# Kernel optimization log

Hardware: AMD Instinct MI355X
Metric: run time of the kernel (lower is better)

Reference implementation:

```python
import jax, jax.numpy as jnp
import numpy as np

N = 100000   # nodes
E = 300000   # directed edges
NG = 4096    # graphs in batch
F_IN = 22
HID = 128


def setup_inputs() -> dict:
    key = jax.random.key(0)
    ks = jax.random.split(key, 32)
    s = 0.05
    inp = {
        "x": jax.random.normal(ks[0], (N, F_IN), jnp.float32),
        "edge_index": jax.random.randint(ks[1], (2, E), 0, N),
        "batch": jnp.sort(jax.random.randint(ks[2], (N,), 0, NG)),
        # GAT layer 1: 22 -> 4 heads x 32
        "W1": jax.random.normal(ks[3], (F_IN, HID), jnp.float32) * s,
        "as1": jax.random.normal(ks[4], (4, 32), jnp.float32) * s,
        "ad1": jax.random.normal(ks[5], (4, 32), jnp.float32) * s,
        "b1": jnp.zeros((HID,), jnp.float32),
        "g1": jnp.ones((HID,), jnp.float32),
        "be1": jnp.zeros((HID,), jnp.float32),
        # GAT layer 2: 128 -> 4 heads x 32
        "W2": jax.random.normal(ks[6], (HID, HID), jnp.float32) * s,
        "as2": jax.random.normal(ks[7], (4, 32), jnp.float32) * s,
        "ad2": jax.random.normal(ks[8], (4, 32), jnp.float32) * s,
        "b2": jnp.zeros((HID,), jnp.float32),
        "g2": jnp.ones((HID,), jnp.float32),
        "be2": jnp.zeros((HID,), jnp.float32),
        # GAT layer 3: 128 -> 1 head x 128
        "W3": jax.random.normal(ks[9], (HID, HID), jnp.float32) * s,
        "as3": jax.random.normal(ks[10], (1, HID), jnp.float32) * s,
        "ad3": jax.random.normal(ks[11], (1, HID), jnp.float32) * s,
        "b3": jnp.zeros((HID,), jnp.float32),
        "g3": jnp.ones((HID,), jnp.float32),
        "be3": jnp.zeros((HID,), jnp.float32),
        # MLP head
        "fw1": jax.random.normal(ks[12], (HID, 64), jnp.float32) * s,
        "fb1": jnp.zeros((64,), jnp.float32),
        "fw2": jax.random.normal(ks[13], (64, 1), jnp.float32) * s,
        "fb2": jnp.zeros((1,), jnp.float32),
    }
    return inp


def reference(x, edge_index, batch, W1, as1, ad1, b1, g1, be1,
              W2, as2, ad2, b2, g2, be2, W3, as3, ad3, b3, g3, be3,
              fw1, fb1, fw2, fb2):
    n = x.shape[0]
    sl = jnp.arange(n)
    src = jnp.concatenate([edge_index[0], sl])  # PyG GATConv adds self-loops
    dst = jnp.concatenate([edge_index[1], sl])

    def gat(h_in, W, a_s, a_d, b):
        H, C = a_s.shape
        h = (h_in @ W).reshape(n, H, C)                      # [N,H,C]
        al_s = jnp.einsum('nhc,hc->nh', h, a_s)              # per-node src score
        al_d = jnp.einsum('nhc,hc->nh', h, a_d)
        e = jax.nn.leaky_relu(al_s[src] + al_d[dst], 0.2)    # [Etot,H]
        emax = jax.ops.segment_max(e, dst, num_segments=n)
        ex = jnp.exp(e - emax[dst])
        den = jax.ops.segment_sum(ex, dst, num_segments=n)
        alpha = ex / (den[dst] + 1e-16)                       # segment softmax over in-edges
        msg = h[src] * alpha[:, :, None]                      # [Etot,H,C]
        out = jax.ops.segment_sum(msg, dst, num_segments=n)
        return out.reshape(n, H * C) + b

    def bn(h, g, be):
        m = h.mean(0)
        v = h.var(0)
        return (h - m) * jax.lax.rsqrt(v + 1e-5) * g + be

    h = jax.nn.relu(bn(gat(x, W1, as1, ad1, b1), g1, be1))
    h = jax.nn.relu(bn(gat(h, W2, as2, ad2, b2), g2, be2))
    h = jax.nn.relu(bn(gat(h, W3, as3, ad3, b3), g3, be3))

    # global mean pool over graphs
    s = jax.ops.segment_sum(h, batch, num_segments=NG)
    cnt = jax.ops.segment_sum(jnp.ones((n,), h.dtype), batch, num_segments=NG)
    pooled = s / jnp.maximum(cnt, 1.0)[:, None]

    z = jax.nn.relu(pooled @ fw1 + fb1)
    return z @ fw2 + fb2
```

## Files before the change

### kernel.cpp

```cpp
#include <hip/hip_runtime.h>

#define N_NODES 100000
#define N_EDGES 300000
#define N_ETOT  400000
#define NGRAPH  4096
#define HID     128
#define NBLK_SCAN 391
#define PNPB    32
#define STATS_BLOCKS 512
#define NSLICE  64

typedef __attribute__((ext_vector_type(8))) short short8;
typedef __attribute__((ext_vector_type(8))) ushort ushort8;
typedef __attribute__((ext_vector_type(4))) float f32x4;

__device__ __forceinline__ ushort f2bf(float f) {
    union { float f; unsigned u; } x; x.f = f;
    unsigned r = x.u + 0x7FFF + ((x.u >> 16) & 1);
    return (ushort)(r >> 16);
}

__device__ __forceinline__ float bf2f(ushort v) {
    union { unsigned u; float f; } t;
    t.u = ((unsigned)v) << 16;
    return t.f;
}

__device__ __forceinline__ float2 bf2f2(unsigned v) {
    union { unsigned u; float f; } lo, hi;
    lo.u = v << 16;
    hi.u = v & 0xFFFF0000u;
    return make_float2(lo.f, hi.f);
}

__global__ __launch_bounds__(256) void setup_kernel(
    const float* __restrict__ x,
    const float* __restrict__ W1, const float* __restrict__ W2, const float* __restrict__ W3,
    ushort* __restrict__ Wt1, ushort* __restrict__ Wt2, ushort* __restrict__ Wt3,
    ushort* __restrict__ Xb, float* __restrict__ sums_sl, int* __restrict__ counts,
    float* __restrict__ pooled)
{
    const int i = blockIdx.x * 256 + threadIdx.x;
    if (i < 16384) {
        int c = i >> 7, k = i & 127;
        Wt2[c * 128 + k] = f2bf(W2[k * 128 + c]);
    } else if (i < 32768) {
        int j = i - 16384; int c = j >> 7, k = j & 127;
        Wt3[c * 128 + k] = f2bf(W3[k * 128 + c]);
    } else if (i < 36864) {
        int j = i - 32768; int c = j >> 5, k = j & 31;
        Wt1[c * 32 + k] = (k < 22) ? f2bf(W1[k * 128 + c]) : (ushort)0;
    } else if (i < 36864 + N_NODES * 32) {
        int j = i - 36864; int n = j >> 5, k = j & 31;
        Xb[j] = (k < 22) ? f2bf(x[n * 22 + k]) : (ushort)0;
    } else if (i < 36864 + N_NODES * 32 + NSLICE * 256) {
        sums_sl[i - (36864 + N_NODES * 32)] = 0.f;
    } else if (i < 36864 + N_NODES * 32 + NSLICE * 256 + N_NODES) {
        counts[i - (36864 + N_NODES * 32 + NSLICE * 256)] = 0;
    } else if (i < 36864 + N_NODES * 32 + NSLICE * 256 + N_NODES + NGRAPH * HID + NGRAPH) {
        pooled[i - (36864 + N_NODES * 32 + NSLICE * 256 + N_NODES)] = 0.f;
    }
}
#define SETUP_TOT (36864 + N_NODES * 32 + NSLICE * 256 + N_NODES + NGRAPH * HID + NGRAPH)

template<int K, bool PRE_BN, int HH>
__global__ __launch_bounds__(256) void mfma_gemm_kernel(
    const ushort* __restrict__ Ab, const ushort* __restrict__ Wt,
    const float* __restrict__ scale, const float* __restrict__ shift,
    const float* __restrict__ avs, const float* __restrict__ avd,
    ushort* __restrict__ Cb, float* __restrict__ als, float* __restrict__ ald, int M)
{
    constexpr int BK  = 32;
    constexpr int LDK = 40;
    constexpr int NT  = K / BK;
    __shared__ ushort Asm[128 * LDK];
    __shared__ ushort Bsm[128 * LDK];
    __shared__ float  ps[128][4], pd[128][4];

    const int tid  = threadIdx.x;
    const int wave = tid >> 6;
    const int lane = tid & 63;
    const int ln   = lane & 15;
    const int quad = lane >> 4;
    const int wr0  = (wave >> 1) * 64;
    const int wc0  = (wave & 1) * 64;
    const int row0 = blockIdx.x * 128;

    f32x4 acc[4][4] = {};

    for (int t = 0; t < NT; ++t) {
        const int k0 = t * BK;
        #pragma unroll
        for (int q = 0; q < 2; ++q) {
            const int chunk = tid + q * 256;
            const int r = chunk >> 2, seg = chunk & 3;
            short8 v = *(const short8*)&Ab[(size_t)(row0 + r) * K + k0 + seg * 8];
            if constexpr (PRE_BN) {
                const int cc = k0 + seg * 8;
                #pragma unroll
                for (int i = 0; i < 8; ++i) {
                    float f = bf2f((ushort)v[i]);
                    f = fmaxf(f * scale[cc + i] + shift[cc + i], 0.f);
                    v[i] = (short)f2bf(f);
                }
            }
            *(short8*)&Asm[r * LDK + seg * 8] = v;
        }
        #pragma unroll
        for (int q = 0; q < 2; ++q) {
            const int chunk = tid + q * 256;
            const int c = chunk >> 2, seg = chunk & 3;
            short8 v = *(const short8*)&Wt[(size_t)c * K + k0 + seg * 8];
            *(short8*)&Bsm[c * LDK + seg * 8] = v;
        }
        __syncthreads();
        short8 af[4], bf[4];
        #pragma unroll
        for (int i = 0; i < 4; ++i) {
            af[i] = *(const short8*)&Asm[(wr0 + i * 16 + ln) * LDK + quad * 8];
            bf[i] = *(const short8*)&Bsm[(wc0 + i * 16 + ln) * LDK + quad * 8];
        }
        #pragma unroll
        for (int tr = 0; tr < 4; ++tr)
            #pragma unroll
            for (int tc = 0; tc < 4; ++tc)
                acc[tr][tc] = __builtin_amdgcn_mfma_f32_16x16x32_bf16(
                    af[tr], bf[tc], acc[tr][tc], 0, 0, 0);
        __syncthreads();
    }

    #pragma unroll
    for (int tr = 0; tr < 4; ++tr)
        #pragma unroll
        for (int rg = 0; rg < 4; ++rg) {
            const int gr = row0 + wr0 + tr * 16 + quad * 4 + rg;
            if (gr < M) {
                #pragma unroll
                for (int tc = 0; tc < 4; ++tc)
                    Cb[(size_t)gr * HID + wc0 + tc * 16 + ln] = f2bf(acc[tr][tc][rg]);
            }
        }

    #pragma unroll
    for (int tr = 0; tr < 4; ++tr)
      #pragma unroll
      for (int rg = 0; rg < 4; ++rg) {
        float sA = 0.f, sB = 0.f, dA = 0.f, dB = 0.f;
        #pragma unroll
        for (int tc = 0; tc < 4; ++tc) {
            const int col = wc0 + tc * 16 + ln;
            const float v = acc[tr][tc][rg];
            if (tc < 2) { sA += v * avs[col]; dA += v * avd[col]; }
            else        { sB += v * avs[col]; dB += v * avd[col]; }
        }
        #pragma unroll
        for (int m = 1; m < 16; m <<= 1) {
            sA += __shfl_xor(sA, m); sB += __shfl_xor(sB, m);
            dA += __shfl_xor(dA, m); dB += __shfl_xor(dB, m);
        }
        if (ln == 0) {
            const int rl = wr0 + tr * 16 + quad * 4 + rg;
            const int h0 = (wave & 1) * 2;
            ps[rl][h0] = sA; ps[rl][h0 + 1] = sB;
            pd[rl][h0] = dA; pd[rl][h0 + 1] = dB;
        }
      }
    __syncthreads();
    {
        const int r  = tid & 127;
        const int gr = row0 + r;
        if (gr < M) {
            if (tid < 128) {
                if (HH == 4) {
                    #pragma unroll
                    for (int h = 0; h < 4; ++h) als[gr * 4 + h] = ps[r][h];
                } else als[gr] = ps[r][0] + ps[r][1] + ps[r][2] + ps[r][3];
            } else {
                if (HH == 4) {
                    #pragma unroll
                    for (int h = 0; h < 4; ++h) ald[gr * 4 + h] = pd[r][h];
                } else ald[gr] = pd[r][0] + pd[r][1] + pd[r][2] + pd[r][3];
            }
        }
    }
}

__global__ void hist_kernel(const int* __restrict__ ei, int* __restrict__ counts) {
    int e = blockIdx.x * blockDim.x + threadIdx.x;
    if (e >= N_ETOT) return;
    int dst = (e < N_EDGES) ? ei[N_EDGES + e] : e - N_EDGES;
    atomicAdd(&counts[dst], 1);
}

__global__ __launch_bounds__(256) void scanA_kernel(
    const int* __restrict__ counts, int* __restrict__ rowptr, int* __restrict__ bsum)
{
    __shared__ int ls[256];
    const int t = threadIdx.x;
    const int i = blockIdx.x * 256 + t;
    const int v = (i < N_NODES) ? counts[i] : 0;
    ls[t] = v; __syncthreads();
    #pragma unroll
    for (int off = 1; off < 256; off <<= 1) {
        int add = (t >= off) ? ls[t - off] : 0;
        __syncthreads();
        ls[t] += add;
        __syncthreads();
    }
    if (i < N_NODES) rowptr[i] = ls[t] - v;
    if (t == 255) bsum[blockIdx.x] = ls[255];
}

__global__ __launch_bounds__(512) void scanB_kernel(int* __restrict__ bsum)
{
    __shared__ int ls[512];
    const int t = threadIdx.x;
    const int v = (t < NBLK_SCAN) ? bsum[t] : 0;
    ls[t] = v; __syncthreads();
    #pragma unroll
    for (int off = 1; off < 512; off <<= 1) {
        int add = (t >= off) ? ls[t - off] : 0;
        __syncthreads();
        ls[t] += add;
        __syncthreads();
    }
    if (t < NBLK_SCAN) bsum[t] = ls[t] - v;
}

__global__ void scanC_kernel(int* __restrict__ rowptr, const int* __restrict__ bsum,
                             int* __restrict__ cursor)
{
    int i = blockIdx.x * 256 + threadIdx.x;
    if (i < N_NODES) {
        int v = rowptr[i] + bsum[blockIdx.x];
        rowptr[i] = v;
        cursor[i] = v;
    }
    if (i == 0) rowptr[N_NODES] = N_ETOT;
}

__global__ void scatter_kernel(const int* __restrict__ ei, int* __restrict__ cursor,
                               int* __restrict__ psrc)
{
    int e = blockIdx.x * blockDim.x + threadIdx.x;
    if (e >= N_ETOT) return;
    int src, dst;
    if (e < N_EDGES) { src = ei[e]; dst = ei[N_EDGES + e]; }
    else             { src = dst = e - N_EDGES; }
    int pos = atomicAdd(&cursor[dst], 1);
    psrc[pos] = src;
}

template<int HH>
__global__ __launch_bounds__(256) void agg_kernel(
    const ushort* __restrict__ H, const float* __restrict__ als,
    const float* __restrict__ ald, const int* __restrict__ rowptr,
    const int* __restrict__ psrc, ushort* __restrict__ Outb)
{
    const int tid  = threadIdx.x;
    const int node = blockIdx.x * 4 + (tid >> 6);
    const int lane = tid & 63;
    const int grp  = lane >> 4;
    const int cl   = lane & 15;
    const int hd   = (HH == 4) ? (cl >> 2) : 0;
    const int r0 = rowptr[node];
    const int r1 = rowptr[node + 1];
    const float aldh = (HH == 4) ? ald[node * 4 + hd] : ald[node];

    float den = 0.f;
    float acc[8] = {};
    for (int p = r0 + grp; p < r1; p += 4) {
        const int src = psrc[p];
        float v = ((HH == 4) ? als[src * 4 + hd] : als[src]) + aldh;
        v = (v > 0.f) ? v : 0.2f * v;
        const float ex = __expf(v);
        const uint4 hv = *(const uint4*)&H[(size_t)src * HID + cl * 8];
        const float2 h0 = bf2f2(hv.x), h1 = bf2f2(hv.y);
        const float2 h2 = bf2f2(hv.z), h3 = bf2f2(hv.w);
        acc[0] += ex * h0.x; acc[1] += ex * h0.y;
        acc[2] += ex * h1.x; acc[3] += ex * h1.y;
        acc[4] += ex * h2.x; acc[5] += ex * h2.y;
        acc[6] += ex * h3.x; acc[7] += ex * h3.y;
        den += ex;
    }
    #pragma unroll
    for (int m = 16; m < 64; m <<= 1) {
        den += __shfl_xor(den, m);
        #pragma unroll
        for (int i = 0; i < 8; ++i) acc[i] += __shfl_xor(acc[i], m);
    }
    if (grp == 0) {
        const float inv = 1.f / (den + 1e-16f);
        ushort8 o;
        #pragma unroll
        for (int i = 0; i < 8; ++i) o[i] = f2bf(acc[i] * inv);
        *(ushort8*)&Outb[(size_t)node * HID + cl * 8] = o;
    }
}

__global__ __launch_bounds__(256) void bn_stats_kernel(
    const ushort* __restrict__ X, float* __restrict__ sums_sl)
{
    __shared__ float ls[16][128], lq[16][128];
    const int tid = threadIdx.x;
    const int ro  = tid >> 4;
    const int ci  = tid & 15;
    const int c0  = ci * 8;
    const int rpb = (N_NODES + STATS_BLOCKS - 1) / STATS_BLOCKS;
    const int r0  = blockIdx.x * rpb;
    const int r1  = min(r0 + rpb, N_NODES);

    float s[8] = {}, q[8] = {};
    for (int r = r0 + ro; r < r1; r += 16) {
        const ushort8 v = *(const ushort8*)&X[(size_t)r * HID + c0];
        #pragma unroll
        for (int j = 0; j < 8; ++j) {
            const float f = bf2f(v[j]);
            s[j] += f; q[j] += f * f;
        }
    }
    #pragma unroll
    for (int j = 0; j < 8; ++j) { ls[ro][c0 + j] = s[j]; lq[ro][c0 + j] = q[j]; }
    __syncthreads();
    const int half = tid >> 7;
    const int c    = tid & 127;
    float acc = 0.f;
    if (half == 0) {
        #pragma unroll
        for (int k = 0; k < 16; ++k) acc += ls[k][c];
    } else {
        #pragma unroll
        for (int k = 0; k < 16; ++k) acc += lq[k][c];
    }
    atomicAdd(&sums_sl[(blockIdx.x & (NSLICE - 1)) * 256 + tid], acc);
}

__global__ __launch_bounds__(256) void bn_finalize_kernel(
    float* __restrict__ sums_sl,
    const float* __restrict__ g, const float* __restrict__ be,
    float* __restrict__ scale, float* __restrict__ shift)
{
    __shared__ float red[256];
    const int tid = threadIdx.x;
    float s = 0.f;
    for (int b = 0; b < NSLICE; ++b) {
        s += sums_sl[b * 256 + tid];
        sums_sl[b * 256 + tid] = 0.f;
    }
    red[tid] = s;
    __syncthreads();
    if (tid < 128) {
        const float m = red[tid] * (1.f / N_NODES);
        const float v = red[tid + 128] * (1.f / N_NODES) - m * m;
        const float sc = g[tid] * rsqrtf(v + 1e-5f);
        scale[tid] = sc;
        shift[tid] = be[tid] - m * sc;
    }
}

__global__ __launch_bounds__(128) void bn_pool_kernel(
    const ushort* __restrict__ X, const float* __restrict__ scale, const float* __restrict__ shift,
    const int* __restrict__ batch, float* __restrict__ pooled, float* __restrict__ cnt)
{
    const int c = threadIdx.x;
    const int n0 = blockIdx.x * PNPB;
    const int n1 = min(n0 + PNPB, N_NODES);
    const float sc = scale[c], sh = shift[c];
    int gcur = batch[n0];
    float acc = 0.f;
    int run = 0;
    for (int n = n0; n < n1; ++n) {
        const int g = batch[n];
        if (g != gcur) {
            atomicAdd(&pooled[(size_t)gcur * HID + c], acc);
            if (c == 0) atomicAdd(&cnt[gcur], (float)run);
            acc = 0.f; run = 0; gcur = g;
        }
        const float v = bf2f(X[(size_t)n * HID + c]) * sc + sh;
        acc += fmaxf(v, 0.f);
        ++run;
    }
    atomicAdd(&pooled[(size_t)gcur * HID + c], acc);
    if (c == 0) atomicAdd(&cnt[gcur], (float)run);
}

__global__ __launch_bounds__(256) void mlp_kernel(
    const float* __restrict__ pooled, const float* __restrict__ cnt,
    const float* __restrict__ fw1, const float* __restrict__ fb1,
    const float* __restrict__ fw2, const float* __restrict__ fb2,
    float* __restrict__ out)
{
    __shared__ float w1[HID * 64];
    __shared__ float rows[4][HID];
    const int tid = threadIdx.x;
    for (int i = tid; i < HID * 64; i += 256) w1[i] = fw1[i];
    const int gl = tid >> 6;
    const int j  = tid & 63;
    const float b1 = fb1[j];
    const float w2 = fw2[j];
    __syncthreads();
    #pragma unroll
    for (int it = 0; it < 4; ++it) {
        const int g = blockIdx.x * 16 + it * 4 + gl;
        const float inv = 1.f / fmaxf(cnt[g], 1.f);
        rows[gl][j]      = pooled[(size_t)g * HID + j] * inv;
        rows[gl][j + 64] = pooled[(size_t)g * HID + 64 + j] * inv;
        __syncthreads();
        float z = b1;
        #pragma unroll 8
        for (int c2 = 0; c2 < HID; ++c2) z += rows[gl][c2] * w1[c2 * 64 + j];
        z = fmaxf(z, 0.f);
        float p = z * w2;
        #pragma unroll
        for (int off = 32; off; off >>= 1) p += __shfl_down(p, off);
        if (j == 0) out[g] = p + fb2[0];
        __syncthreads();
    }
}

extern "C" void kernel_launch(void* const* d_in, const int* in_sizes, int n_in,
                              void* d_out, int out_size, void* d_ws, size_t ws_size,
                              hipStream_t stream)
{
    const float* x     = (const float*)d_in[0];
    const int*   ei    = (const int*)d_in[1];
    const int*   batch = (const int*)d_in[2];
    const float* W1  = (const float*)d_in[3];
    const float* as1 = (const float*)d_in[4];
    const float* ad1 = (const float*)d_in[5];
    const float* g1  = (const float*)d_in[7];
    const float* be1 = (const float*)d_in[8];
    const float* W2  = (const float*)d_in[9];
    const float* as2 = (const float*)d_in[10];
    const float* ad2 = (const float*)d_in[11];
    const float* g2  = (const float*)d_in[13];
    const float* be2 = (const float*)d_in[14];
    const float* W3  = (const float*)d_in[15];
    const float* as3 = (const float*)d_in[16];
    const float* ad3 = (const float*)d_in[17];
    const float* g3  = (const float*)d_in[19];
    const float* be3 = (const float*)d_in[20];
    const float* fw1 = (const float*)d_in[21];
    const float* fb1 = (const float*)d_in[22];
    const float* fw2 = (const float*)d_in[23];
    const float* fb2 = (const float*)d_in[24];
    float* out = (float*)d_out;

    ushort* Hb  = (ushort*)d_ws;
    ushort* Bh  = Hb  + (size_t)N_NODES * HID;
    ushort* Xb  = Bh  + (size_t)N_NODES * HID;
    ushort* Wt1 = Xb  + (size_t)N_NODES * 32;
    ushort* Wt2 = Wt1 + 128 * 32;
    ushort* Wt3 = Wt2 + 128 * 128;
    float* als    = (float*)(Wt3 + 128 * 128);
    float* ald    = als + (size_t)N_NODES * 4;
    float* sums_sl= ald + (size_t)N_NODES * 4;
    float* scale  = sums_sl + NSLICE * 256;
    float* shift  = scale + HID;
    float* pooled = shift + HID;
    float* cnt    = pooled + (size_t)NGRAPH * HID;
    int*   rowptr = (int*)(cnt + NGRAPH);
    int*   counts = rowptr + (N_NODES + 1);
    int*   cursor = counts + N_NODES;
    int*   bsum   = cursor + N_NODES;
    int*   psrc   = bsum + 512;

    auto cdiv = [](int a, int b) { return (a + b - 1) / b; };

    setup_kernel<<<cdiv(SETUP_TOT, 256), 256, 0, stream>>>(
        x, W1, W2, W3, Wt1, Wt2, Wt3, Xb, sums_sl, counts, pooled);

    hist_kernel<<<cdiv(N_ETOT, 256), 256, 0, stream>>>(ei, counts);
    scanA_kernel<<<NBLK_SCAN, 256, 0, stream>>>(counts, rowptr, bsum);
    scanB_kernel<<<1, 512, 0, stream>>>(bsum);
    scanC_kernel<<<NBLK_SCAN, 256, 0, stream>>>(rowptr, bsum, cursor);
    scatter_kernel<<<cdiv(N_ETOT, 256), 256, 0, stream>>>(ei, cursor, psrc);

    const int ggrid = cdiv(N_NODES, 128);
    const int agrid = N_NODES / 4;

    mfma_gemm_kernel<32, false, 4><<<ggrid, 256, 0, stream>>>(
        Xb, Wt1, nullptr, nullptr, as1, ad1, Hb, als, ald, N_NODES);
    agg_kernel<4><<<agrid, 256, 0, stream>>>(Hb, als, ald, rowptr, psrc, Bh);
    bn_stats_kernel<<<STATS_BLOCKS, 256, 0, stream>>>(Bh, sums_sl);
    bn_finalize_kernel<<<1, 256, 0, stream>>>(sums_sl, g1, be1, scale, shift);

    mfma_gemm_kernel<128, true, 4><<<ggrid, 256, 0, stream>>>(
        Bh, Wt2, scale, shift, as2, ad2, Hb, als, ald, N_NODES);
    agg_kernel<4><<<agrid, 256, 0, stream>>>(Hb, als, ald, rowptr, psrc, Bh);
    bn_stats_kernel<<<STATS_BLOCKS, 256, 0, stream>>>(Bh, sums_sl);
    bn_finalize_kernel<<<1, 256, 0, stream>>>(sums_sl, g2, be2, scale, shift);

    mfma_gemm_kernel<128, true, 1><<<ggrid, 256, 0, stream>>>(
        Bh, Wt3, scale, shift, as3, ad3, Hb, als, ald, N_NODES);
    agg_kernel<1><<<agrid, 256, 0, stream>>>(Hb, als, ald, rowptr, psrc, Bh);
    bn_stats_kernel<<<STATS_BLOCKS, 256, 0, stream>>>(Bh, sums_sl);
    bn_finalize_kernel<<<1, 256, 0, stream>>>(sums_sl, g3, be3, scale, shift);

    bn_pool_kernel<<<cdiv(N_NODES, PNPB), 128, 0, stream>>>(Bh, scale, shift, batch, pooled, cnt);
    mlp_kernel<<<NGRAPH / 16, 256, 0, stream>>>(pooled, cnt, fw1, fb1, fw2, fb2, out);
}
```

Measured before the change: 382.3 us.

## Load full K panel into XOR-swizzled LDS once, dropping per-k-step barriers

The GEMM kernel now loads the entire K-width A and W panels into shared memory in a single pass, issuing all global loads up front before the BN/ReLU prologue. This removes the per-BK-step loop and its two barriers per iteration. An XOR swizzle on the 16-byte segment index replaces the padded stride to avoid LDS bank conflicts. The score scratch arrays reuse the A/B LDS buffers after an added barrier. LDS use grows to 64 KB for K=128, which may reduce occupancy.

```diff
diff --git a/kernel.cpp b/kernel.cpp
--- a/kernel.cpp
+++ b/kernel.cpp
@@ -70,12 +70,14 @@
     const float* __restrict__ avs, const float* __restrict__ avd,
     ushort* __restrict__ Cb, float* __restrict__ als, float* __restrict__ ald, int M)
 {
-    constexpr int BK  = 32;
-    constexpr int LDK = 40;
-    constexpr int NT  = K / BK;
-    __shared__ ushort Asm[128 * LDK];
-    __shared__ ushort Bsm[128 * LDK];
-    __shared__ float  ps[128][4], pd[128][4];
+    constexpr int SEGS = K / 8;
+    constexpr int SSH  = (K == 128) ? 4 : 2;
+    constexpr int SWM  = SEGS - 1;
+    constexpr int NP   = SEGS / 2;
+    constexpr int KT   = K / 32;
+
+    __shared__ ushort Asm[128 * K];
+    __shared__ ushort Bsm[128 * K];
 
     const int tid  = threadIdx.x;
     const int wave = tid >> 6;
@@ -86,39 +88,49 @@
     const int wc0  = (wave & 1) * 64;
     const int row0 = blockIdx.x * 128;
 
+    short8 aR[NP], wR[NP];
+    #pragma unroll
+    for (int q = 0; q < NP; ++q) {
+        const int chunk = tid + q * 256;
+        const int r   = chunk >> SSH;
+        const int seg = chunk & SWM;
+        aR[q] = *(const short8*)&Ab[(size_t)(row0 + r) * K + seg * 8];
+        wR[q] = *(const short8*)&Wt[(size_t)r * K + seg * 8];
+    }
+    if constexpr (PRE_BN) {
+        #pragma unroll
+        for (int q = 0; q < NP; ++q) {
+            const int seg = (tid + q * 256) & SWM;
+            const int cc  = seg * 8;
+            #pragma unroll
+            for (int i = 0; i < 8; ++i) {
+                float f = bf2f((ushort)aR[q][i]);
+                f = fmaxf(f * scale[cc + i] + shift[cc + i], 0.f);
+                aR[q][i] = (short)f2bf(f);
+            }
+        }
+    }
+    #pragma unroll
+    for (int q = 0; q < NP; ++q) {
+        const int chunk = tid + q * 256;
+        const int r   = chunk >> SSH;
+        const int seg = chunk & SWM;
+        const int sp  = seg ^ (r & SWM);
+        *(short8*)&Asm[r * K + sp * 8] = aR[q];
+        *(short8*)&Bsm[r * K + sp * 8] = wR[q];
+    }
+    __syncthreads();
+
     f32x4 acc[4][4] = {};
-
-    for (int t = 0; t < NT; ++t) {
-        const int k0 = t * BK;
-        #pragma unroll
-        for (int q = 0; q < 2; ++q) {
-            const int chunk = tid + q * 256;
-            const int r = chunk >> 2, seg = chunk & 3;
-            short8 v = *(const short8*)&Ab[(size_t)(row0 + r) * K + k0 + seg * 8];
-            if constexpr (PRE_BN) {
-                const int cc = k0 + seg * 8;
-                #pragma unroll
-                for (int i = 0; i < 8; ++i) {
-                    float f = bf2f((ushort)v[i]);
-                    f = fmaxf(f * scale[cc + i] + shift[cc + i], 0.f);
-                    v[i] = (short)f2bf(f);
-                }
-            }
-            *(short8*)&Asm[r * LDK + seg * 8] = v;
-        }
-        #pragma unroll
-        for (int q = 0; q < 2; ++q) {
-            const int chunk = tid + q * 256;
-            const int c = chunk >> 2, seg = chunk & 3;
-            short8 v = *(const short8*)&Wt[(size_t)c * K + k0 + seg * 8];
-            *(short8*)&Bsm[c * LDK + seg * 8] = v;
-        }
-        __syncthreads();
+    #pragma unroll
+    for (int kt = 0; kt < KT; ++kt) {
         short8 af[4], bf[4];
         #pragma unroll
         for (int i = 0; i < 4; ++i) {
-            af[i] = *(const short8*)&Asm[(wr0 + i * 16 + ln) * LDK + quad * 8];
-            bf[i] = *(const short8*)&Bsm[(wc0 + i * 16 + ln) * LDK + quad * 8];
+            const int ra = wr0 + i * 16 + ln;
+            const int ca = wc0 + i * 16 + ln;
+            af[i] = *(const short8*)&Asm[ra * K + (((kt * 4 + quad) ^ (ra & SWM)) * 8)];
+            bf[i] = *(const short8*)&Bsm[ca * K + (((kt * 4 + quad) ^ (ca & SWM)) * 8)];
         }
         #pragma unroll
         for (int tr = 0; tr < 4; ++tr)
@@ -126,7 +138,6 @@
             for (int tc = 0; tc < 4; ++tc)
                 acc[tr][tc] = __builtin_amdgcn_mfma_f32_16x16x32_bf16(
                     af[tr], bf[tc], acc[tr][tc], 0, 0, 0);
-        __syncthreads();
     }
 
     #pragma unroll
@@ -141,6 +152,9 @@
             }
         }
 
+    __syncthreads();
+    float* ps = (float*)Asm;
+    float* pd = (float*)Bsm;
     #pragma unroll
     for (int tr = 0; tr < 4; ++tr)
       #pragma unroll
@@ -161,8 +175,8 @@
         if (ln == 0) {
             const int rl = wr0 + tr * 16 + quad * 4 + rg;
             const int h0 = (wave & 1) * 2;
-            ps[rl][h0] = sA; ps[rl][h0 + 1] = sB;
-            pd[rl][h0] = dA; pd[rl][h0 + 1] = dB;
+            ps[rl * 4 + h0] = sA; ps[rl * 4 + h0 + 1] = sB;
+            pd[rl * 4 + h0] = dA; pd[rl * 4 + h0 + 1] = dB;
         }
       }
     __syncthreads();
@@ -173,13 +187,13 @@
             if (tid < 128) {
                 if (HH == 4) {
                     #pragma unroll
-                    for (int h = 0; h < 4; ++h) als[gr * 4 + h] = ps[r][h];
-                } else als[gr] = ps[r][0] + ps[r][1] + ps[r][2] + ps[r][3];
+                    for (int h = 0; h < 4; ++h) als[gr * 4 + h] = ps[r * 4 + h];
+                } else als[gr] = ps[r * 4] + ps[r * 4 + 1] + ps[r * 4 + 2] + ps[r * 4 + 3];
             } else {
                 if (HH == 4) {
                     #pragma unroll
-                    for (int h = 0; h < 4; ++h) ald[gr * 4 + h] = pd[r][h];
-                } else ald[gr] = pd[r][0] + pd[r][1] + pd[r][2] + pd[r][3];
+                    for (int h = 0; h < 4; ++h) ald[gr * 4 + h] = pd[r * 4 + h];
+                } else ald[gr] = pd[r * 4] + pd[r * 4 + 1] + pd[r * 4 + 2] + pd[r * 4 + 3];
             }
         }
     }
```

Result: faster. 366.4 us (median of 2 runs) (-4.1%).
